# Kernel optimization log

Hardware: AMD Instinct MI355X
Metric: run time of the kernel (lower is better)

## Reference

```python
import jax, jax.numpy as jnp
import numpy as np

B, L, HID = 2, 2048, 512
NUM_HEADS = 8
HEAD_DIM = HID // NUM_HEADS
GAP_ROWS = 33   # num_time_gap_buckets + 1
DUR_ROWS = 17   # num_duration_buckets + 1
NEG = -1e9      # finite stand-in for -inf (grad-safe, masked probs ~0)


def setup_inputs() -> dict:
    key = jax.random.key(0)
    ks = jax.random.split(key, 16)
    s = 1.0 / np.sqrt(HID)
    x = jax.random.normal(ks[0], (B, L, HID), dtype=jnp.float32)
    attention_mask = jax.random.randint(ks[1], (B, L), 0, 2, dtype=jnp.int32)
    time_gap_bucket_ids = jax.random.randint(ks[2], (B, L), 0, GAP_ROWS, dtype=jnp.int32)
    duration_bucket_ids = jax.random.randint(ks[3], (B, L), 0, DUR_ROWS, dtype=jnp.int32)
    Wq = jax.random.normal(ks[4], (HID, HID), dtype=jnp.float32) * s
    bq = jnp.zeros((HID,), jnp.float32)
    Wk = jax.random.normal(ks[5], (HID, HID), dtype=jnp.float32) * s
    bk = jnp.zeros((HID,), jnp.float32)
    Wv = jax.random.normal(ks[6], (HID, HID), dtype=jnp.float32) * s
    bv = jnp.zeros((HID,), jnp.float32)
    Wo = jax.random.normal(ks[7], (HID, HID), dtype=jnp.float32) * s
    bo = jnp.zeros((HID,), jnp.float32)
    # bias tables: padding_idx=0 row kept at zero, rest random for a meaningful test
    gap_emb = jax.random.normal(ks[8], (GAP_ROWS, NUM_HEADS), dtype=jnp.float32) * 0.1
    gap_emb = gap_emb.at[0].set(0.0)
    dur_emb = jax.random.normal(ks[9], (DUR_ROWS, NUM_HEADS), dtype=jnp.float32) * 0.1
    dur_emb = dur_emb.at[0].set(0.0)
    return dict(x=x, attention_mask=attention_mask,
                time_gap_bucket_ids=time_gap_bucket_ids,
                duration_bucket_ids=duration_bucket_ids,
                Wq=Wq, bq=bq, Wk=Wk, bk=bk, Wv=Wv, bv=bv, Wo=Wo, bo=bo,
                gap_emb=gap_emb, dur_emb=dur_emb)


def reference(x, attention_mask, time_gap_bucket_ids, duration_bucket_ids,
              Wq, bq, Wk, bk, Wv, bv, Wo, bo, gap_emb, dur_emb):
    b, l, hid = x.shape
    h, d = NUM_HEADS, HEAD_DIM
    def split_heads(t):  # (B,L,HID) -> (B,h,L,d)
        return t.reshape(b, l, h, d).transpose(0, 2, 1, 3)
    Q = split_heads(x @ Wq + bq)
    K = split_heads(x @ Wk + bk)
    V = split_heads(x @ Wv + bv)
    scores = jnp.einsum('bhqd,bhkd->bhqk', Q, K) / jnp.sqrt(jnp.float32(d))
    # relative time-gap bias: (B,L,L) bucket lookup -> (B,h,L,L)
    rel = jnp.abs(time_gap_bucket_ids[:, :, None] - time_gap_bucket_ids[:, None, :])
    rel = jnp.clip(rel, 0, GAP_ROWS - 1)
    gap_bias = gap_emb[rel]                       # (B,L,L,h)
    scores = scores + gap_bias.transpose(0, 3, 1, 2)
    # per-key duration bias: (B,L,h) -> (B,h,1,L)
    dur_bias = dur_emb[duration_bucket_ids]       # (B,L,h)
    scores = scores + dur_bias.transpose(0, 2, 1)[:, :, None, :]
    pad = (attention_mask == 0)[:, None, None, :]  # (B,1,1,L) over keys
    scores = jnp.where(pad, NEG, scores)
    attn = jax.nn.softmax(scores, axis=-1)
    out = jnp.einsum('bhqk,bhkd->bhqd', attn, V)
    out = out.transpose(0, 2, 1, 3).reshape(b, l, hid)
    return out @ Wo + bo
```

## Files before the change

### kernel.cpp

```cpp
#include <hip/hip_runtime.h>
#include <cmath>

typedef unsigned short u16;
typedef unsigned int   u32;
typedef __attribute__((ext_vector_type(2))) unsigned uintx2;
typedef __attribute__((ext_vector_type(4))) float    floatx4;
typedef __attribute__((ext_vector_type(4))) unsigned uintx4;
typedef __attribute__((ext_vector_type(8))) __bf16   bf16x8;

#define MFMA16(a, b, c) __builtin_amdgcn_mfma_f32_16x16x32_bf16((a), (b), (c), 0, 0, 0)

__device__ __forceinline__ u16 f2bf(float f) {
    union { float f; u32 u; } v; v.f = f;
    u32 u = v.u;
    return (u16)((u + 0x7FFFu + ((u >> 16) & 1u)) >> 16);
}
__device__ __forceinline__ float bfhi2f(u32 u) {
    return __builtin_bit_cast(float, u & 0xFFFF0000u);
}
__device__ __forceinline__ float bflo2f(u32 u) {
    return __builtin_bit_cast(float, u << 16);
}

__device__ __forceinline__ bf16x8 ld_frag(const u16* p) {
    uintx4 t = *(const uintx4*)p;
    return __builtin_bit_cast(bf16x8, t);
}

#if __has_builtin(__builtin_amdgcn_exp2f)
#define EXP2F(x) __builtin_amdgcn_exp2f(x)
#else
#define EXP2F(x) exp2f(x)
#endif

typedef __attribute__((address_space(3))) unsigned       lds_u32;
typedef __attribute__((address_space(1))) const unsigned glb_u32;
__device__ __forceinline__ void gl_lds16(const void* g, void* l) {
    __builtin_amdgcn_global_load_lds((glb_u32*)(uintptr_t)g, (lds_u32*)(uintptr_t)l, 16, 0, 0);
}

#define DRAIN() asm volatile("s_waitcnt vmcnt(0)" ::: "memory")

#define LOG2E   1.4426950408889634f
#define QSCALE  0.18033688011112043f

__global__ __launch_bounds__(256) void prep_kernel(
        const float* __restrict__ x, const int* __restrict__ gap_ids,
        const int* __restrict__ dur_ids, const int* __restrict__ amask,
        const float* __restrict__ gap_emb, const float* __restrict__ dur_emb,
        const float* __restrict__ Wq, const float* __restrict__ Wk,
        const float* __restrict__ Wv, const float* __restrict__ Wo,
        u16* __restrict__ Xb, u16* __restrict__ Qe, u16* __restrict__ Ke,
        u16* __restrict__ WqT, u16* __restrict__ WkT,
        u16* __restrict__ WvT, u16* __restrict__ WoT) {
    __shared__ u16 T[64][72];
    int bid = blockIdx.x, tid = threadIdx.x;
    if (bid < 1024) {
        int idx = bid * 256 + tid;
        const float* src = x + (size_t)idx * 8;
        uintx4 o;
        o.x = f2bf(src[0]) | ((u32)f2bf(src[1]) << 16);
        o.y = f2bf(src[2]) | ((u32)f2bf(src[3]) << 16);
        o.z = f2bf(src[4]) | ((u32)f2bf(src[5]) << 16);
        o.w = f2bf(src[6]) | ((u32)f2bf(src[7]) << 16);
        *(uintx4*)(Xb + (size_t)idx * 8) = o;
    } else if (bid < 2048) {
        int ri = (bid - 1024) * 32 + (tid >> 3);
        int l = ri & 2047;
        int b = ri >> 14;
        int ch = tid & 7;
        int gq = gap_ids[b * 2048 + l];
        u16 lg = f2bf(LOG2E);
        u16 vals[8];
        for (int e = 0; e < 8; e++) {
            int j = ch * 8 + e;
            vals[e] = (j == gq || j == 33) ? lg : (u16)0;
        }
        *(uintx4*)(Qe + (size_t)ri * 128 + (8 + ch) * 8) = *(uintx4*)vals;
    } else if (bid < 3072) {
        int ri = (bid - 2048) * 32 + (tid >> 3);
        int bh = ri >> 11, l = ri & 2047;
        int b = bh >> 3, h = bh & 7;
        int ch = tid & 7;
        int gk = gap_ids[b * 2048 + l];
        int did = dur_ids[b * 2048 + l];
        int msk = amask[b * 2048 + l];
        float kval = msk ? dur_emb[did * 8 + h] : -1e9f;
        u16 vals[8];
        for (int e = 0; e < 8; e++) {
            int j = ch * 8 + e;
            float v;
            if (j <= 32) { int d = j - gk; d = d < 0 ? -d : d; v = gap_emb[d * 8 + h]; }
            else if (j == 33) v = kval;
            else v = 0.f;
            vals[e] = f2bf(v);
        }
        int phys = 8 | (ch ^ (l & 7));
        *(uintx4*)(Ke + (size_t)ri * 128 + phys * 8) = *(uintx4*)vals;
    } else {
        int bid2 = bid - 3072;
        int mat = bid2 >> 6, t8 = bid2 & 63;
        int n0 = (t8 & 7) * 64, k0 = (t8 >> 3) * 64;
        const float* W = (mat == 0) ? Wq : (mat == 1) ? Wk : (mat == 2) ? Wv : Wo;
        u16* WT = (mat == 0) ? WqT : (mat == 1) ? WkT : (mat == 2) ? WvT : WoT;
        int r = tid >> 4, cq = tid & 15;
        for (int rr = 0; rr < 4; rr++) {
            int row = r + rr * 16;
            floatx4 s = *(const floatx4*)&W[(size_t)(k0 + row) * 512 + n0 + cq * 4];
            T[cq * 4 + 0][row] = f2bf(s.x);
            T[cq * 4 + 1][row] = f2bf(s.y);
            T[cq * 4 + 2][row] = f2bf(s.z);
            T[cq * 4 + 3][row] = f2bf(s.w);
        }
        __syncthreads();
        for (int p = 0; p < 2; p++) {
            int idx = p * 256 + tid;
            int c = idx >> 3, ch = idx & 7;
            *(uintx4*)&WT[(size_t)(n0 + c) * 512 + k0 + ch * 8] = *(const uintx4*)&T[c][ch * 8];
        }
    }
}

__global__ __launch_bounds__(256) void gemm_qkv(
        const u16* __restrict__ Xb,
        const u16* __restrict__ WqT, const u16* __restrict__ WkT, const u16* __restrict__ WvT,
        const float* __restrict__ bq, const float* __restrict__ bk, const float* __restrict__ bv,
        u16* __restrict__ Qe, u16* __restrict__ Ke, u16* __restrict__ Vt) {
    __shared__ u16 smem[2][16384];

    int tid = threadIdx.x;
    int m0 = blockIdx.x * 128;
    int gy = blockIdx.y;
    int mat = gy >> 2, hp = gy & 3;
    int ncol0 = hp * 128;
    const u16* Bt = (mat == 0) ? WqT : (mat == 1) ? WkT : WvT;
    const float* bias = (mat == 0) ? bq : (mat == 1) ? bk : bv;

    int lane = tid & 63, w = tid >> 6, lo = lane & 15, hi = lane >> 4;
    int wm = w >> 1, wn = w & 1;
    floatx4 acc[4][4] = {};

#define QSTAGE(KB, BUF) do {                                                            \
        int k0_ = (KB) * 64;                                                            \
        for (int it = 0; it < 4; it++) {                                                \
            int c = it * 256 + tid;                                                     \
            int row = c >> 3, ch = c & 7;                                               \
            gl_lds16((const char*)Xb + ((size_t)(m0 + row) * 512 + k0_) * 2 + ch * 16,  \
                     (char*)(smem[BUF]) + c * 16);                                      \
        }                                                                               \
        for (int it = 0; it < 4; it++) {                                                \
            int c = it * 256 + tid;                                                     \
            int row = c >> 3, ch = c & 7;                                               \
            gl_lds16((const char*)Bt + ((size_t)(ncol0 + row) * 512 + k0_) * 2 + ch * 16,\
                     (char*)(smem[BUF] + 8192) + c * 16);                               \
        }                                                                               \
    } while (0)

    QSTAGE(0, 0);
    for (int kb = 0; kb < 8; kb++) {
        DRAIN();
        __syncthreads();
        if (kb + 1 < 8) QSTAGE(kb + 1, (kb + 1) & 1);
        const u16* As = smem[kb & 1];
        const u16* Bs = smem[kb & 1] + 8192;
        for (int s = 0; s < 2; s++) {
            bf16x8 a[4], b[4];
            for (int i = 0; i < 4; i++)
                a[i] = ld_frag(&As[(64 * wm + 16 * i + lo) * 64 + s * 32 + hi * 8]);
            for (int j = 0; j < 4; j++)
                b[j] = ld_frag(&Bs[(64 * wn + 16 * j + lo) * 64 + s * 32 + hi * 8]);
            for (int i = 0; i < 4; i++)
                for (int j = 0; j < 4; j++)
                    acc[i][j] = MFMA16(a[i], b[j], acc[i][j]);
        }
    }
#undef QSTAGE

    int bb = m0 >> 11, l0 = m0 & 2047;
    __syncthreads();

    if (mat < 2) {
        u16* Ot = &smem[0][0];
        for (int j = 0; j < 4; j++) {
            int c64 = 16 * j + lo;
            float bval = bias[ncol0 + 64 * wn + c64];
            for (int i = 0; i < 4; i++) {
                int row = 64 * wm + 16 * i + 4 * hi;
                for (int r = 0; r < 4; r++) {
                    float v = acc[i][j][r] + bval;
                    if (mat == 0) v *= QSCALE;
                    Ot[(row + r) * 144 + wn * 72 + c64] = f2bf(v);
                }
            }
        }
        __syncthreads();
        for (int p = 0; p < 8; p++) {
            int cc = p * 256 + tid;
            int row = cc >> 4, hcb = cc & 15;
            int h2 = hcb >> 3, ch = hcb & 7;
            int lrow = l0 + row;
            size_t rowi = (size_t)(bb * 8 + 2 * hp + h2) * 2048 + lrow;
            int ch2 = (mat == 1) ? (ch ^ (lrow & 7)) : ch;
            u16* dstp = (mat == 0) ? Qe : Ke;
            *(uintx4*)(dstp + rowi * 128 + ch2 * 8) =
                *(const uintx4*)(Ot + row * 144 + h2 * 72 + ch * 8);
        }
    } else {
        u16* Ot = &smem[0][0];
        for (int j = 0; j < 4; j++) {
            int dcs = 64 * wn + 16 * j + lo;
            float bval = bias[ncol0 + dcs];
            for (int i = 0; i < 4; i++) {
                int row = 64 * wm + 16 * i + 4 * hi;
                for (int r = 0; r < 4; r++)
                    Ot[dcs * 136 + row + r] = f2bf(acc[i][j][r] + bval);
            }
        }
        __syncthreads();
        for (int p = 0; p < 8; p++) {
            int cc4 = p * 256 + tid;
            int dcs = cc4 >> 4, c16 = cc4 & 15;
            int g64 = c16 >> 3, phys = c16 & 7;
            int h2 = dcs >> 6, dc = dcs & 63;
            int mlog = phys ^ (dc & 7);
            int g = mlog >> 2, q = mlog & 3;
            int base = g64 * 64 + 32 * g + 4 * q;
            uintx2 lo4 = *(const uintx2*)(Ot + dcs * 136 + base);
            uintx2 hi4 = *(const uintx2*)(Ot + dcs * 136 + base + 16);
            uintx4 t; t.x = lo4.x; t.y = lo4.y; t.z = hi4.x; t.w = hi4.y;
            size_t dst = ((size_t)(bb * 8 + 2 * hp + h2) * 64 + dc) * 2048
                         + l0 + g64 * 64 + phys * 8;
            *(uintx4*)(Vt + dst) = t;
        }
    }
}

__global__ __launch_bounds__(256, 3) void flash_attn(
        const u16* __restrict__ Qe, const u16* __restrict__ Ke, const u16* __restrict__ Vt,
        u16* __restrict__ Opart, float* __restrict__ Lpart) {
    __shared__ u16 Ks[2][64 * 128];
    __shared__ u16 Vs[2][64 * 64];

    int tid = threadIdx.x, lane = tid & 63, w = tid >> 6, lo = lane & 15, hi = lane >> 4;
    int qt2 = blockIdx.x, bh = blockIdx.y, sp = blockIdx.z;
    int sw = lo & 7;

    bf16x8 bq_[2][4];
    for (int g = 0; g < 2; g++) {
        size_t qrow = ((size_t)bh * 2048 + qt2 * 128 + g * 64 + 16 * w + lo) * 128;
        for (int kc = 0; kc < 4; kc++) bq_[g][kc] = ld_frag(&Qe[qrow + kc * 32 + hi * 8]);
    }

    floatx4 O[2][4] = {};
    floatx4 Lacc[2] = {};
    uintx4 onesu; onesu.x = 0x3F803F80u; onesu.y = 0x3F803F80u; onesu.z = 0x3F803F80u; onesu.w = 0x3F803F80u;
    bf16x8 ones = __builtin_bit_cast(bf16x8, onesu);

    const u16* KeB = Ke + (size_t)bh * 2048 * 128;
    const u16* VtB = Vt + (size_t)bh * 64 * 2048;

    int kbeg = sp * 16, kend = kbeg + 16;

#define STAGE(KT, BUF) do {                                                        \
        int k0_ = (KT) * 64;                                                       \
        const char* gk_ = (const char*)(KeB + (size_t)k0_ * 128);                  \
        char* lk_ = (char*)Ks[BUF];                                                \
        for (int r2 = 0; r2 < 4; r2++)                                             \
            gl_lds16(gk_ + r2 * 4096 + tid * 16, lk_ + r2 * 4096 + tid * 16);      \
        for (int p2 = 0; p2 < 2; p2++) {                                           \
            int c_ = p2 * 256 + tid;                                               \
            int row_ = c_ >> 3, ch_ = c_ & 7;                                      \
            gl_lds16((const char*)(VtB + (size_t)row_ * 2048 + k0_) + ch_ * 16,    \
                     (char*)Vs[BUF] + c_ * 16);                                    \
        }                                                                          \
    } while (0)

    int cur = 0;
    STAGE(kbeg, 0);
    for (int kt = kbeg; kt < kend; kt++) {
        DRAIN();
        __syncthreads();
        if (kt + 1 < kend) STAGE(kt + 1, cur ^ 1);

        const u16* Ksc = Ks[cur];
        const u16* Vsc = Vs[cur];

        floatx4 sf[2][4] = {};
        for (int t = 0; t < 4; t++) {
            const u16* krow = &Ksc[(16 * t + lo) * 128];
            for (int kc = 0; kc < 4; kc++) {
                int cc = kc * 4 + hi;
                int pc = (cc & 8) | ((cc & 7) ^ sw);
                bf16x8 a = ld_frag(&krow[pc * 8]);
                sf[0][t] = MFMA16(a, bq_[0][kc], sf[0][t]);
                sf[1][t] = MFMA16(a, bq_[1][kc], sf[1][t]);
            }
        }

        bf16x8 af[2][2];
        for (int g = 0; g < 2; g++) {
            u32 pk[4][2];
            for (int t = 0; t < 4; t++) {
                float p0 = EXP2F(sf[g][t][0]);
                float p1 = EXP2F(sf[g][t][1]);
                float p2 = EXP2F(sf[g][t][2]);
                float p3 = EXP2F(sf[g][t][3]);
                u32 u0 = __builtin_bit_cast(u32, p0) + 0x8000u;
                u32 u1 = __builtin_bit_cast(u32, p1) + 0x8000u;
                u32 u2 = __builtin_bit_cast(u32, p2) + 0x8000u;
                u32 u3 = __builtin_bit_cast(u32, p3) + 0x8000u;
                pk[t][0] = __builtin_amdgcn_perm(u1, u0, 0x07060302);
                pk[t][1] = __builtin_amdgcn_perm(u3, u2, 0x07060302);
            }
            for (int tp = 0; tp < 2; tp++) {
                uintx4 av;
                av.x = pk[2 * tp][0]; av.y = pk[2 * tp][1];
                av.z = pk[2 * tp + 1][0]; av.w = pk[2 * tp + 1][1];
                af[g][tp] = __builtin_bit_cast(bf16x8, av);
            }
        }

        for (int tp = 0; tp < 2; tp++) {
            Lacc[0] = MFMA16(af[0][tp], ones, Lacc[0]);
            Lacc[1] = MFMA16(af[1][tp], ones, Lacc[1]);
            for (int u = 0; u < 4; u++) {
                const u16* vrow = &Vsc[(16 * u + lo) * 64];
                int m = (4 * tp + hi) ^ sw;
                bf16x8 bv = ld_frag(&vrow[m * 8]);
                O[0][u] = MFMA16(af[0][tp], bv, O[0][u]);
                O[1][u] = MFMA16(af[1][tp], bv, O[1][u]);
            }
        }
        cur ^= 1;
    }
#undef STAGE

    for (int g = 0; g < 2; g++) {
        int qt = 2 * qt2 + g;
        size_t obase = (((size_t)sp * 16 + bh) * 32 + qt) * 4096;
        for (int u = 0; u < 4; u++)
            for (int r = 0; r < 4; r++)
                Opart[obase + (size_t)(16 * w + 4 * hi + r) * 64 + 16 * u + lo] =
                    f2bf(O[g][u][r]);
        if (lo == 0) {
            size_t lbase = (((size_t)sp * 16 + bh) * 32 + qt) * 64;
            for (int r = 0; r < 4; r++) Lpart[lbase + 16 * w + 4 * hi + r] = Lacc[g][r];
        }
    }
}

__global__ __launch_bounds__(256) void combine_kernel(const u16* __restrict__ Opart,
                                                      const float* __restrict__ Lpart,
                                                      u16* __restrict__ Ob) {
    int idx = blockIdx.x * 256 + threadIdx.x;
    int d4 = idx & 15;
    int q = (idx >> 4) & 2047;
    int bh = idx >> 15;
    int qt = q >> 6, qr = q & 63;
    size_t b0 = ((size_t)bh * 32 + qt) * 4096 + qr * 64 + d4 * 4;
    uintx2 a0 = *(const uintx2*)&Opart[b0];
    uintx2 a1 = *(const uintx2*)&Opart[b0 + 2097152];
    size_t lb = ((size_t)bh * 32 + qt) * 64 + qr;
    float rl = 1.0f / (Lpart[lb] + Lpart[lb + 32768]);
    float s0 = bflo2f(a0.x) + bflo2f(a1.x);
    float s1 = bfhi2f(a0.x) + bfhi2f(a1.x);
    float s2 = bflo2f(a0.y) + bflo2f(a1.y);
    float s3 = bfhi2f(a0.y) + bfhi2f(a1.y);
    uintx2 pk2;
    pk2.x = f2bf(s0 * rl) | ((u32)f2bf(s1 * rl) << 16);
    pk2.y = f2bf(s2 * rl) | ((u32)f2bf(s3 * rl) << 16);
    int bb = bh >> 3, h = bh & 7;
    *(uintx2*)&Ob[((size_t)(bb * 2048 + q)) * 512 + h * 64 + d4 * 4] = pk2;
}

__global__ __launch_bounds__(256) void gemm_out(
        const u16* __restrict__ Ob, const u16* __restrict__ WoT,
        const float* __restrict__ bo, float* __restrict__ out) {
    __shared__ u16 smem[2][8192];
    int tid = threadIdx.x;
    int m0 = blockIdx.x * 64;
    int n0 = blockIdx.y * 64;
    int lane = tid & 63, w = tid >> 6, lo = lane & 15, hi = lane >> 4;
    floatx4 acc[4] = {};

#define OSTAGE(KB, BUF) do {                                                            \
        int k0_ = (KB) * 64;                                                            \
        for (int it = 0; it < 2; it++) {                                                \
            int c = it * 256 + tid;                                                     \
            int row = c >> 3, ch = c & 7;                                               \
            gl_lds16((const char*)Ob + ((size_t)(m0 + row) * 512 + k0_) * 2 + ch * 16,  \
                     (char*)(smem[BUF]) + c * 16);                                      \
        }                                                                               \
        for (int it = 0; it < 2; it++) {                                                \
            int c = it * 256 + tid;                                                     \
            int row = c >> 3, ch = c & 7;                                               \
            gl_lds16((const char*)WoT + ((size_t)(n0 + row) * 512 + k0_) * 2 + ch * 16, \
                     (char*)(smem[BUF] + 4096) + c * 16);                               \
        }                                                                               \
    } while (0)

    OSTAGE(0, 0);
    for (int kb = 0; kb < 8; kb++) {
        DRAIN();
        __syncthreads();
        if (kb + 1 < 8) OSTAGE(kb + 1, (kb + 1) & 1);
        const u16* As = smem[kb & 1];
        const u16* Bs = smem[kb & 1] + 4096;
        for (int s = 0; s < 2; s++) {
            bf16x8 a = ld_frag(&As[(16 * w + lo) * 64 + s * 32 + hi * 8]);
            for (int t = 0; t < 4; t++) {
                bf16x8 b = ld_frag(&Bs[(16 * t + lo) * 64 + s * 32 + hi * 8]);
                acc[t] = MFMA16(a, b, acc[t]);
            }
        }
    }
#undef OSTAGE

    for (int t = 0; t < 4; t++) {
        int n = n0 + 16 * t + lo;
        float bval = bo[n];
        for (int r = 0; r < 4; r++) {
            int mrow = m0 + 16 * w + 4 * hi + r;
            out[(size_t)mrow * 512 + n] = acc[t][r] + bval;
        }
    }
}

extern "C" void kernel_launch(void* const* d_in, const int* in_sizes, int n_in,
                              void* d_out, int out_size, void* d_ws, size_t ws_size,
                              hipStream_t stream) {
    const float* x     = (const float*)d_in[0];
    const int*   amask = (const int*)d_in[1];
    const int*   gids  = (const int*)d_in[2];
    const int*   dids  = (const int*)d_in[3];
    const float* Wq    = (const float*)d_in[4];
    const float* bq    = (const float*)d_in[5];
    const float* Wk    = (const float*)d_in[6];
    const float* bk    = (const float*)d_in[7];
    const float* Wv    = (const float*)d_in[8];
    const float* bv    = (const float*)d_in[9];
    const float* Wo    = (const float*)d_in[10];
    const float* bo    = (const float*)d_in[11];
    const float* gap_emb = (const float*)d_in[12];
    const float* dur_emb = (const float*)d_in[13];
    float* out = (float*)d_out;

    char* ws = (char*)d_ws;
    u16*   Qe    = (u16*)(ws + 0);
    u16*   Ke    = (u16*)(ws + 8388608);
    u16*   Vt    = (u16*)(ws + 16777216);
    u16*   Opart = (u16*)(ws + 20971520);
    float* Lpart = (float*)(ws + 29360128);
    u16*   Ob    = (u16*)(ws + 29622272);
    u16*   WoT   = (u16*)(ws + 33816576);
    u16*   Xb    = (u16*)(ws + 20971520);
    u16*   WqT   = (u16*)(ws + 25165824);
    u16*   WkT   = (u16*)(ws + 25690112);
    u16*   WvT   = (u16*)(ws + 26214400);

    hipLaunchKernelGGL(prep_kernel, dim3(3328), dim3(256), 0, stream,
                       x, gids, dids, amask, gap_emb, dur_emb,
                       Wq, Wk, Wv, Wo, Xb, Qe, Ke, WqT, WkT, WvT, WoT);
    hipLaunchKernelGGL(gemm_qkv, dim3(32, 12), dim3(256), 0, stream,
                       Xb, WqT, WkT, WvT, bq, bk, bv, Qe, Ke, Vt);
    hipLaunchKernelGGL(flash_attn, dim3(16, 16, 2), dim3(256), 0, stream,
                       Qe, Ke, Vt, Opart, Lpart);
    hipLaunchKernelGGL(combine_kernel, dim3(2048), dim3(256), 0, stream,
                       Opart, Lpart, Ob);
    hipLaunchKernelGGL(gemm_out, dim3(64, 8), dim3(256), 0, stream,
                       Ob, WoT, bo, out);
}
```

Before: 140.8 us.

## Fuse split-K attention combine into output projection GEMM

Removes the separate combine kernel and the Ob intermediate buffer. The output GEMM now reads both partial attention outputs and their softmax denominators directly, normalizes and sums them in registers, and writes the A tile to shared memory per k-block, while Wo tiles stay double-buffered. This saves a launch and a global write/read of the combined output. In exchange, each of the 8 N-blocks recomputes the combine, which multiplies Opart reads eightfold, and an extra barrier is added per iteration. Workspace offsets are relaid out.

```diff
diff --git a/kernel.cpp b/kernel.cpp
--- a/kernel.cpp
+++ b/kernel.cpp
@@ -349,72 +349,82 @@
     }
 }
 
-__global__ __launch_bounds__(256) void combine_kernel(const u16* __restrict__ Opart,
-                                                      const float* __restrict__ Lpart,
-                                                      u16* __restrict__ Ob) {
-    int idx = blockIdx.x * 256 + threadIdx.x;
-    int d4 = idx & 15;
-    int q = (idx >> 4) & 2047;
-    int bh = idx >> 15;
-    int qt = q >> 6, qr = q & 63;
-    size_t b0 = ((size_t)bh * 32 + qt) * 4096 + qr * 64 + d4 * 4;
-    uintx2 a0 = *(const uintx2*)&Opart[b0];
-    uintx2 a1 = *(const uintx2*)&Opart[b0 + 2097152];
-    size_t lb = ((size_t)bh * 32 + qt) * 64 + qr;
-    float rl = 1.0f / (Lpart[lb] + Lpart[lb + 32768]);
-    float s0 = bflo2f(a0.x) + bflo2f(a1.x);
-    float s1 = bfhi2f(a0.x) + bfhi2f(a1.x);
-    float s2 = bflo2f(a0.y) + bflo2f(a1.y);
-    float s3 = bfhi2f(a0.y) + bfhi2f(a1.y);
-    uintx2 pk2;
-    pk2.x = f2bf(s0 * rl) | ((u32)f2bf(s1 * rl) << 16);
-    pk2.y = f2bf(s2 * rl) | ((u32)f2bf(s3 * rl) << 16);
-    int bb = bh >> 3, h = bh & 7;
-    *(uintx2*)&Ob[((size_t)(bb * 2048 + q)) * 512 + h * 64 + d4 * 4] = pk2;
-}
-
-__global__ __launch_bounds__(256) void gemm_out(
-        const u16* __restrict__ Ob, const u16* __restrict__ WoT,
-        const float* __restrict__ bo, float* __restrict__ out) {
-    __shared__ u16 smem[2][8192];
+__global__ __launch_bounds__(256) void gemm_out_fused(
+        const u16* __restrict__ Opart, const float* __restrict__ Lpart,
+        const u16* __restrict__ WoT, const float* __restrict__ bo,
+        float* __restrict__ out) {
+    __shared__ u16 As[4096];
+    __shared__ u16 Bs[2][4096];
+
     int tid = threadIdx.x;
     int m0 = blockIdx.x * 64;
     int n0 = blockIdx.y * 64;
     int lane = tid & 63, w = tid >> 6, lo = lane & 15, hi = lane >> 4;
+    int bb = m0 >> 11, qt = (m0 & 2047) >> 6;
+    int qr = tid >> 2, dbase = (tid & 3) * 16;
     floatx4 acc[4] = {};
 
-#define OSTAGE(KB, BUF) do {                                                            \
+#define BSTAGE(KB, BUF) do {                                                            \
         int k0_ = (KB) * 64;                                                            \
         for (int it = 0; it < 2; it++) {                                                \
             int c = it * 256 + tid;                                                     \
             int row = c >> 3, ch = c & 7;                                               \
-            gl_lds16((const char*)Ob + ((size_t)(m0 + row) * 512 + k0_) * 2 + ch * 16,  \
-                     (char*)(smem[BUF]) + c * 16);                                      \
-        }                                                                               \
-        for (int it = 0; it < 2; it++) {                                                \
-            int c = it * 256 + tid;                                                     \
-            int row = c >> 3, ch = c & 7;                                               \
             gl_lds16((const char*)WoT + ((size_t)(n0 + row) * 512 + k0_) * 2 + ch * 16, \
-                     (char*)(smem[BUF] + 4096) + c * 16);                               \
+                     (char*)(Bs[BUF]) + c * 16);                                        \
         }                                                                               \
     } while (0)
 
-    OSTAGE(0, 0);
+    uintx4 ar[2][2];
+    float lv[2];
+#define LOADA(H) do {                                                                   \
+        for (int sp_ = 0; sp_ < 2; sp_++) {                                             \
+            size_t ab = ((size_t)(sp_ * 16 + bb * 8 + (H)) * 32 + qt) * 4096            \
+                        + (size_t)qr * 64 + dbase;                                      \
+            ar[sp_][0] = *(const uintx4*)&Opart[ab];                                    \
+            ar[sp_][1] = *(const uintx4*)&Opart[ab + 8];                                \
+            lv[sp_] = Lpart[((size_t)(sp_ * 16 + bb * 8 + (H)) * 32 + qt) * 64 + qr];   \
+        }                                                                               \
+    } while (0)
+
+    BSTAGE(0, 0);
+    LOADA(0);
+    int cur = 0;
     for (int kb = 0; kb < 8; kb++) {
         DRAIN();
         __syncthreads();
-        if (kb + 1 < 8) OSTAGE(kb + 1, (kb + 1) & 1);
-        const u16* As = smem[kb & 1];
-        const u16* Bs = smem[kb & 1] + 4096;
+
+        float rl = 1.0f / (lv[0] + lv[1]);
+        uintx4 o0, o1;
+        {
+            u32 wds[8];
+            for (int half = 0; half < 2; half++)
+                for (int wd = 0; wd < 4; wd++) {
+                    u32 ua = ar[0][half][wd], ub = ar[1][half][wd];
+                    float sA = bflo2f(ua) + bflo2f(ub);
+                    float sB = bfhi2f(ua) + bfhi2f(ub);
+                    wds[half * 4 + wd] = f2bf(sA * rl) | ((u32)f2bf(sB * rl) << 16);
+                }
+            o0.x = wds[0]; o0.y = wds[1]; o0.z = wds[2]; o0.w = wds[3];
+            o1.x = wds[4]; o1.y = wds[5]; o1.z = wds[6]; o1.w = wds[7];
+        }
+        *(uintx4*)&As[qr * 64 + dbase] = o0;
+        *(uintx4*)&As[qr * 64 + dbase + 8] = o1;
+
+        if (kb + 1 < 8) { BSTAGE(kb + 1, cur ^ 1); LOADA(kb + 1); }
+        __syncthreads();
+
+        const u16* Bsc = Bs[cur];
         for (int s = 0; s < 2; s++) {
             bf16x8 a = ld_frag(&As[(16 * w + lo) * 64 + s * 32 + hi * 8]);
             for (int t = 0; t < 4; t++) {
-                bf16x8 b = ld_frag(&Bs[(16 * t + lo) * 64 + s * 32 + hi * 8]);
+                bf16x8 b = ld_frag(&Bsc[(16 * t + lo) * 64 + s * 32 + hi * 8]);
                 acc[t] = MFMA16(a, b, acc[t]);
             }
         }
-    }
-#undef OSTAGE
+        cur ^= 1;
+    }
+#undef BSTAGE
+#undef LOADA
 
     for (int t = 0; t < 4; t++) {
         int n = n0 + 16 * t + lo;
@@ -451,12 +461,11 @@
     u16*   Vt    = (u16*)(ws + 16777216);
     u16*   Opart = (u16*)(ws + 20971520);
     float* Lpart = (float*)(ws + 29360128);
-    u16*   Ob    = (u16*)(ws + 29622272);
-    u16*   WoT   = (u16*)(ws + 33816576);
-    u16*   Xb    = (u16*)(ws + 20971520);
-    u16*   WqT   = (u16*)(ws + 25165824);
-    u16*   WkT   = (u16*)(ws + 25690112);
-    u16*   WvT   = (u16*)(ws + 26214400);
+    u16*   WoT   = (u16*)(ws + 29622272);
+    u16*   Xb    = (u16*)(ws + 30146560);
+    u16*   WqT   = (u16*)(ws + 34340864);
+    u16*   WkT   = (u16*)(ws + 34865152);
+    u16*   WvT   = (u16*)(ws + 35389440);
 
     hipLaunchKernelGGL(prep_kernel, dim3(3328), dim3(256), 0, stream,
                        x, gids, dids, amask, gap_emb, dur_emb,
@@ -465,8 +474,6 @@
                        Xb, WqT, WkT, WvT, bq, bk, bv, Qe, Ke, Vt);
     hipLaunchKernelGGL(flash_attn, dim3(16, 16, 2), dim3(256), 0, stream,
                        Qe, Ke, Vt, Opart, Lpart);
-    hipLaunchKernelGGL(combine_kernel, dim3(2048), dim3(256), 0, stream,
-                       Opart, Lpart, Ob);
-    hipLaunchKernelGGL(gemm_out, dim3(64, 8), dim3(256), 0, stream,
-                       Ob, WoT, bo, out);
-}
+    hipLaunchKernelGGL(gemm_out_fused, dim3(64, 8), dim3(256), 0, stream,
+                       Opart, Lpart, WoT, bo, out);
+}
```

After: 143.7 us. 1.02x slower.
